# Kernel tuning notes

Measured on AMD Instinct MI355X. Metric: run time of the kernel, lower is better.

## Reference

```python
import jax, jax.numpy as jnp
import numpy as np
from jax import lax

N = 5000          # num atoms
E = 4             # num edge types
DIM_H = 128
VOCAB = 100       # num_atoms_vocab; embedding table has VOCAB+1 rows
T = 4             # max_time_steps


def setup_inputs() -> dict:
    key = jax.random.key(0)
    k1, k2, k3, k4 = jax.random.split(key, 4)
    atom_arr = jax.random.randint(k1, (N,), 0, VOCAB, dtype=jnp.int64 if jax.config.read('jax_enable_x64') else jnp.int32)
    adjs = jax.random.randint(k2, (E, N, N), 0, 2, dtype=jnp.int32)
    # learned parameters
    embedding = jax.random.normal(k3, (VOCAB + 1, DIM_H), dtype=jnp.float32) * 0.05
    limit = float(np.sqrt(6.0 / (DIM_H + DIM_H)))  # glorot uniform
    H_edges = jax.random.uniform(k4, (E, DIM_H, DIM_H), minval=-limit, maxval=limit, dtype=jnp.float32)
    return {
        "atom_arr": atom_arr,
        "adjs": adjs,
        "max_time_steps": T,
        "embedding": embedding,
        "H_edges": H_edges,
    }


def reference(atom_arr, adjs, max_time_steps, embedding, H_edges):
    # h_v^0 = embedding lookup, [N, H]
    h0 = embedding[atom_arr]
    # adjacency mask as float, [E, N, N]
    A = (adjs == 1).astype(h0.dtype)

    def step(h, _):
        # original: for each node v, edge type e: H_e @ sum_{u: adj[e,v,u]==1} h_u
        agg = jnp.einsum('evu,uh->evh', A, h)          # neighbor sum per edge type
        msg = jnp.einsum('eij,evj->vi', H_edges, agg)  # edge-type transform + sum over e
        h_new = jax.nn.sigmoid(h + msg)
        return h_new, h_new

    _, h_all = lax.scan(step, h0, None, length=max_time_steps)
    return h_all  # [T, N, H]
```

## Files before the change

### kernel.cpp

```cpp
#include <hip/hip_runtime.h>

#define NROW 5000
#define NPAD 5120
#define KPAD 5120
#define KW   80
#define KC   80
#define KZ   4
#define KCQ  20
#define HDIM 128
#define MTI  5
#define MROWS (MTI * 32)
#define FXS  4194304.0f
#define PART ((size_t)4 * NROW * HDIM)

typedef _Float16 f16x8 __attribute__((ext_vector_type(8)));
typedef float f32x16 __attribute__((ext_vector_type(16)));

__device__ __forceinline__ unsigned short f2h_int(int v) {
    union { _Float16 h; unsigned short u; } c;
    c.h = (_Float16)(float)v;
    return c.u;
}
__device__ __forceinline__ void fx_digits(float h, unsigned short& d1, unsigned short& d0) {
    int q = (int)rintf(h * FXS);
    d1 = f2h_int(q >> 11);
    d0 = f2h_int(q & 2047);
}

__device__ __forceinline__ size_t bt_idx(int kc, int pl, int kk, int half, int col, int j) {
    return (((((size_t)kc * 2 + pl) * 4 + kk) * 2 + half) * 128 + col) * 8 + j;
}

__global__ __launch_bounds__(256) void prep_atom_kernel(const unsigned int* __restrict__ atomw,
                                                        int* __restrict__ atomIdx) {
    __shared__ int s_is64;
    if (threadIdx.x == 0) {
        bool all0 = true, anynz = false;
        for (int j = 0; j < 64; ++j) {
            unsigned lo = atomw[2 * j], hi = atomw[2 * j + 1];
            all0 = all0 && (hi == 0u);
            anynz = anynz || (lo != 0u);
        }
        s_is64 = (all0 && anynz) ? 1 : 0;
    }
    __syncthreads();
    int v = blockIdx.x * 256 + threadIdx.x;
    if (v < NROW) atomIdx[v] = s_is64 ? (int)atomw[2 * v] : (int)atomw[v];
}

__global__ __launch_bounds__(256) void prep_pack_kernel(const int* __restrict__ adjs,
                                                        unsigned long long* __restrict__ packedT) {
    const int er = blockIdx.x;
    const int e = er / NPAD;
    const int r = er - e * NPAD;
    const int wave = threadIdx.x >> 6;
    const int lane = threadIdx.x & 63;
    const int* rowp = adjs + ((size_t)e * NROW + r) * NROW;
    unsigned long long* outp = packedT + (size_t)e * KC * NPAD + r;
    const bool rok = (r < NROW);
    for (int c = wave; c < KW; c += 4) {
        int u = c * 64 + lane;
        int val = (rok && u < NROW) ? rowp[u] : 0;
        unsigned long long m = __ballot(val == 1);
        if (lane == 0) outp[(size_t)c * NPAD] = m;
    }
}

__global__ __launch_bounds__(256) void prep_h0T_kernel(const int* __restrict__ atomIdx,
                                                       const float* __restrict__ emb,
                                                       unsigned short* __restrict__ hTt) {
    const int i = blockIdx.y;
    const int v = blockIdx.x * 256 + threadIdx.x;
    float val = 0.f;
    if (v < NROW) val = emb[(size_t)atomIdx[v] * HDIM + i];
    unsigned short d1, d0;
    fx_digits(val, d1, d0);
    const int kc = v >> 6, kk = (v >> 4) & 3, half = (v >> 3) & 1, j = v & 7;
    hTt[bt_idx(kc, 0, kk, half, i, j)] = d1;
    hTt[bt_idx(kc, 1, kk, half, i, j)] = d0;
}

__global__ __launch_bounds__(256) void prep_h0f_kernel(const int* __restrict__ atomIdx,
                                                       const float* __restrict__ emb,
                                                       float* __restrict__ h) {
    int idx = blockIdx.x * 256 + threadIdx.x;
    int v = idx >> 7, i = idx & 127;
    h[idx] = emb[(size_t)atomIdx[v] * HDIM + i];
}

__global__ __launch_bounds__(256) void prep_Ht_kernel(const float* __restrict__ H,
                                                      float* __restrict__ Htr) {
    int idx = blockIdx.x * 256 + threadIdx.x;
    int e = idx >> 14;
    int j = (idx >> 7) & 127;
    int i = idx & 127;
    Htr[idx] = H[((size_t)e * HDIM + i) * HDIM + j];
}

__global__ __launch_bounds__(256, 2) void gemm1_kernel(const unsigned long long* __restrict__ packedT,
                                                       const unsigned short* __restrict__ hTt,
                                                       float* __restrict__ agg) {
    const int m0 = blockIdx.x * MROWS;
    const int e = blockIdx.y;
    const int kz = blockIdx.z;
    const int tid = threadIdx.x;
    const int lane = tid & 63;
    const int wave = tid >> 6;
    const int l31 = lane & 31;
    const int l1 = lane >> 5;
    const int sh2 = l1 * 8;
    const int col = wave * 32 + l31;

    f32x16 acc[2][MTI];
#pragma unroll
    for (int pl = 0; pl < 2; ++pl)
#pragma unroll
        for (int mt = 0; mt < MTI; ++mt) acc[pl][mt] = (f32x16)(0.f);

    const int kc0 = kz * KCQ;
    const unsigned long long* ap = packedT + ((size_t)e * KC + kc0) * NPAD + m0 + l31;
    const _Float16* bp = (const _Float16*)hTt + (size_t)kc0 * 16384 + (size_t)l1 * 1024 + (size_t)col * 8;

    for (int kc = 0; kc < KCQ; ++kc) {
        unsigned long long aw[MTI];
#pragma unroll
        for (int mt = 0; mt < MTI; ++mt) aw[mt] = ap[mt * 32];

        f16x8 bf[2][4];
#pragma unroll
        for (int pl = 0; pl < 2; ++pl)
#pragma unroll
            for (int kk = 0; kk < 4; ++kk)
                bf[pl][kk] = *(const f16x8*)(bp + pl * 8192 + kk * 2048);

        ap += NPAD;
        bp += 16384;

#pragma unroll
        for (int kk = 0; kk < 4; ++kk) {
#pragma unroll
            for (int mt = 0; mt < MTI; ++mt) {
                unsigned int w = (kk < 2) ? (unsigned int)aw[mt] : (unsigned int)(aw[mt] >> 32);
                unsigned int b = (w >> ((kk & 1) * 16 + sh2)) & 0xFFu;
                unsigned int y = b | (b << 15);
                union { unsigned int u[4]; f16x8 h; } A;
#pragma unroll
                for (int q = 0; q < 4; ++q)
                    A.u[q] = ((y >> (2 * q)) & 0x00010001u) * 0x3C00u;
#pragma unroll
                for (int pl = 0; pl < 2; ++pl)
                    acc[pl][mt] = __builtin_amdgcn_mfma_f32_32x32x16_f16(
                        A.h, bf[pl][kk], acc[pl][mt], 0, 0, 0);
            }
        }
    }

    float* aggz = agg + (size_t)kz * PART;
#pragma unroll
    for (int mt = 0; mt < MTI; ++mt)
#pragma unroll
        for (int reg = 0; reg < 16; ++reg) {
            int row = (reg & 3) + 8 * (reg >> 2) + 4 * l1;
            int v = m0 + mt * 32 + row;
            if (v < NROW) {
                double d = (double)acc[0][mt][reg] * 2048.0 + (double)acc[1][mt][reg];
                aggz[((size_t)e * NROW + v) * HDIM + col] = (float)(d * (1.0 / 4194304.0));
            }
        }
}

__global__ __launch_bounds__(256) void gemm2_kernel(const float* __restrict__ agg,
                                                    const float* __restrict__ Htr,
                                                    float* __restrict__ h,
                                                    float* __restrict__ outp,
                                                    unsigned short* __restrict__ hTt) {
    __shared__ float aggs[16][512];
    __shared__ unsigned short hs[2][128][16];
    const int v0 = blockIdx.x * 16;
    const int tid = threadIdx.x;

#pragma unroll
    for (int it = 0; it < 8; ++it) {
        int idx = it * 256 + tid;
        int vv = idx >> 7;
        int ej = (idx & 127) * 4;
        int e = ej >> 7, j = ej & 127;
        int v = v0 + vv;
        float4 val = make_float4(0.f, 0.f, 0.f, 0.f);
        if (v < NROW) {
            size_t o = ((size_t)e * NROW + v) * HDIM + j;
            float4 a0 = *(const float4*)&agg[o];
            float4 a1 = *(const float4*)&agg[PART + o];
            float4 a2 = *(const float4*)&agg[2 * PART + o];
            float4 a3 = *(const float4*)&agg[3 * PART + o];
            val = make_float4((a0.x + a1.x) + (a2.x + a3.x), (a0.y + a1.y) + (a2.y + a3.y),
                              (a0.z + a1.z) + (a2.z + a3.z), (a0.w + a1.w) + (a2.w + a3.w));
        }
        *(float4*)&aggs[vv][ej] = val;
    }
    __syncthreads();

    const int i = tid & 127;
    const int vg = tid >> 7;
    float m4[8][4];
#pragma unroll
    for (int vv = 0; vv < 8; ++vv)
#pragma unroll
        for (int k = 0; k < 4; ++k) m4[vv][k] = 0.f;

    for (int c = 0; c < 512; c += 4) {
        float w0 = Htr[(size_t)(c + 0) * HDIM + i];
        float w1 = Htr[(size_t)(c + 1) * HDIM + i];
        float w2 = Htr[(size_t)(c + 2) * HDIM + i];
        float w3 = Htr[(size_t)(c + 3) * HDIM + i];
#pragma unroll
        for (int vv = 0; vv < 8; ++vv) {
            const float4 a = *(const float4*)&aggs[vg * 8 + vv][c];
            m4[vv][0] += a.x * w0;
            m4[vv][1] += a.y * w1;
            m4[vv][2] += a.z * w2;
            m4[vv][3] += a.w * w3;
        }
    }

#pragma unroll
    for (int vv = 0; vv < 8; ++vv) {
        int v = v0 + vg * 8 + vv;
        unsigned short d1 = 0, d0 = 0;
        if (v < NROW) {
            size_t o = (size_t)v * HDIM + i;
            float msg = (m4[vv][0] + m4[vv][1]) + (m4[vv][2] + m4[vv][3]);
            float x = h[o] + msg;
            float s = 1.0f / (1.0f + expf(-x));
            outp[o] = s;
            h[o] = s;
            fx_digits(s, d1, d0);
        }
        hs[0][i][vg * 8 + vv] = d1;
        hs[1][i][vg * 8 + vv] = d0;
    }
    __syncthreads();
    if (tid < 128) {
        const int kc = v0 >> 6, kk = (v0 >> 4) & 3;
#pragma unroll
        for (int pl = 0; pl < 2; ++pl) {
            const uint4* sp = (const uint4*)&hs[pl][tid][0];
            *(uint4*)&hTt[bt_idx(kc, pl, kk, 0, tid, 0)] = sp[0];
            *(uint4*)&hTt[bt_idx(kc, pl, kk, 1, tid, 0)] = sp[1];
        }
    }
}

extern "C" void kernel_launch(void* const* d_in, const int* in_sizes, int n_in,
                              void* d_out, int out_size, void* d_ws, size_t ws_size,
                              hipStream_t stream) {
    const unsigned int* atomw = (const unsigned int*)d_in[0];
    const int* adjs = (const int*)d_in[1];
    const float* emb = (const float*)d_in[3];
    const float* H = (const float*)d_in[4];
    float* out = (float*)d_out;

    char* ws = (char*)d_ws;
    unsigned long long* packedT = (unsigned long long*)ws;
    size_t off = (size_t)4 * KC * NPAD * 8;
    unsigned short* hTt = (unsigned short*)(ws + off);
    off += (size_t)2 * KC * HDIM * 64 * 2;
    float* hf = (float*)(ws + off);
    off += (size_t)NROW * HDIM * 4;
    float* agg = (float*)(ws + off);
    off += (size_t)KZ * PART * 4;
    float* Htr = (float*)(ws + off);
    off += (size_t)4 * HDIM * HDIM * 4;
    int* atomIdx = (int*)(ws + off);
    off += (size_t)NROW * 4;

    prep_atom_kernel<<<dim3((NROW + 255) / 256), 256, 0, stream>>>(atomw, atomIdx);
    prep_pack_kernel<<<dim3(4 * NPAD), 256, 0, stream>>>(adjs, packedT);
    prep_h0T_kernel<<<dim3(KPAD / 256, HDIM), 256, 0, stream>>>(atomIdx, emb, hTt);
    prep_h0f_kernel<<<dim3(NROW * HDIM / 256), 256, 0, stream>>>(atomIdx, emb, hf);
    prep_Ht_kernel<<<dim3(4 * HDIM * HDIM / 256), 256, 0, stream>>>(H, Htr);

    for (int t = 0; t < 4; ++t) {
        gemm1_kernel<<<dim3(NPAD / MROWS, 4, KZ), 256, 0, stream>>>(packedT, hTt, agg);
        gemm2_kernel<<<dim3((NROW + 15) / 16), 256, 0, stream>>>(agg, Htr, hf,
                                                                 out + (size_t)t * NROW * HDIM, hTt);
    }
}
```

Before: 1.057 ms.

## Fuse time-step GEMM kernels into one persistent kernel with grid barriers

```diff
diff --git a/kernel.cpp b/kernel.cpp
--- a/kernel.cpp
+++ b/kernel.cpp
@@ -2,7 +2,6 @@
 
 #define NROW 5000
 #define NPAD 5120
-#define KPAD 5120
 #define KW   80
 #define KC   80
 #define KZ   4
@@ -10,6 +9,8 @@
 #define HDIM 128
 #define MTI  5
 #define MROWS (MTI * 32)
+#define GRID1 512
+#define NT2  625
 #define FXS  4194304.0f
 #define PART ((size_t)4 * NROW * HDIM)
 
@@ -31,8 +32,20 @@
     return (((((size_t)kc * 2 + pl) * 4 + kk) * 2 + half) * 128 + col) * 8 + j;
 }
 
+__device__ __forceinline__ void gridbar(int* bar, int idx) {
+    __syncthreads();
+    if (threadIdx.x == 0) {
+        __hip_atomic_fetch_add(&bar[idx], 1, __ATOMIC_ACQ_REL, __HIP_MEMORY_SCOPE_AGENT);
+        while (__hip_atomic_load(&bar[idx], __ATOMIC_ACQUIRE, __HIP_MEMORY_SCOPE_AGENT) < GRID1)
+            __builtin_amdgcn_s_sleep(2);
+    }
+    __syncthreads();
+}
+
 __global__ __launch_bounds__(256) void prep_atom_kernel(const unsigned int* __restrict__ atomw,
-                                                        int* __restrict__ atomIdx) {
+                                                        int* __restrict__ atomIdx,
+                                                        int* __restrict__ bar) {
+    if (blockIdx.x == 0 && threadIdx.x < 16) bar[threadIdx.x] = 0;
     __shared__ int s_is64;
     if (threadIdx.x == 0) {
         bool all0 = true, anynz = false;
@@ -97,157 +110,174 @@
     Htr[idx] = H[((size_t)e * HDIM + i) * HDIM + j];
 }
 
-__global__ __launch_bounds__(256, 2) void gemm1_kernel(const unsigned long long* __restrict__ packedT,
-                                                       const unsigned short* __restrict__ hTt,
-                                                       float* __restrict__ agg) {
-    const int m0 = blockIdx.x * MROWS;
-    const int e = blockIdx.y;
-    const int kz = blockIdx.z;
+__global__ __launch_bounds__(256, 2) void fused_kernel(const unsigned long long* __restrict__ packedT,
+                                                       unsigned short* __restrict__ hTt,
+                                                       float* __restrict__ agg,
+                                                       const float* __restrict__ Htr,
+                                                       float* __restrict__ hf,
+                                                       float* __restrict__ out,
+                                                       int* __restrict__ bar) {
+    __shared__ float aggs[8][512];
+    __shared__ unsigned short hs[2][128][8];
     const int tid = threadIdx.x;
+    const int bid = blockIdx.x;
+
+    const int mblk = bid & 31;
+    const int e1 = (bid >> 5) & 3;
+    const int kz = bid >> 7;
     const int lane = tid & 63;
     const int wave = tid >> 6;
     const int l31 = lane & 31;
     const int l1 = lane >> 5;
     const int sh2 = l1 * 8;
     const int col = wave * 32 + l31;
-
-    f32x16 acc[2][MTI];
-#pragma unroll
-    for (int pl = 0; pl < 2; ++pl)
-#pragma unroll
-        for (int mt = 0; mt < MTI; ++mt) acc[pl][mt] = (f32x16)(0.f);
-
+    const int m0 = mblk * MROWS;
     const int kc0 = kz * KCQ;
-    const unsigned long long* ap = packedT + ((size_t)e * KC + kc0) * NPAD + m0 + l31;
-    const _Float16* bp = (const _Float16*)hTt + (size_t)kc0 * 16384 + (size_t)l1 * 1024 + (size_t)col * 8;
-
-    for (int kc = 0; kc < KCQ; ++kc) {
-        unsigned long long aw[MTI];
-#pragma unroll
-        for (int mt = 0; mt < MTI; ++mt) aw[mt] = ap[mt * 32];
-
-        f16x8 bf[2][4];
-#pragma unroll
-        for (int pl = 0; pl < 2; ++pl)
-#pragma unroll
-            for (int kk = 0; kk < 4; ++kk)
-                bf[pl][kk] = *(const f16x8*)(bp + pl * 8192 + kk * 2048);
-
-        ap += NPAD;
-        bp += 16384;
-
-#pragma unroll
-        for (int kk = 0; kk < 4; ++kk) {
-#pragma unroll
-            for (int mt = 0; mt < MTI; ++mt) {
-                unsigned int w = (kk < 2) ? (unsigned int)aw[mt] : (unsigned int)(aw[mt] >> 32);
-                unsigned int b = (w >> ((kk & 1) * 16 + sh2)) & 0xFFu;
-                unsigned int y = b | (b << 15);
-                union { unsigned int u[4]; f16x8 h; } A;
-#pragma unroll
-                for (int q = 0; q < 4; ++q)
-                    A.u[q] = ((y >> (2 * q)) & 0x00010001u) * 0x3C00u;
+
+    const int ip = tid & 63;
+    const int vg = tid >> 6;
+    const int i0 = ip * 2;
+
+    for (int t = 0; t < 4; ++t) {
+        {
+            f32x16 acc[2][MTI];
+#pragma unroll
+            for (int pl = 0; pl < 2; ++pl)
+#pragma unroll
+                for (int mt = 0; mt < MTI; ++mt) acc[pl][mt] = (f32x16)(0.f);
+
+            const unsigned long long* ap = packedT + ((size_t)e1 * KC + kc0) * NPAD + m0 + l31;
+            const _Float16* bp = (const _Float16*)hTt + (size_t)kc0 * 16384 +
+                                 (size_t)l1 * 1024 + (size_t)col * 8;
+
+            for (int kc = 0; kc < KCQ; ++kc) {
+                unsigned long long aw[MTI];
+#pragma unroll
+                for (int mt = 0; mt < MTI; ++mt) aw[mt] = ap[mt * 32];
+
+                f16x8 bf[2][4];
 #pragma unroll
                 for (int pl = 0; pl < 2; ++pl)
-                    acc[pl][mt] = __builtin_amdgcn_mfma_f32_32x32x16_f16(
-                        A.h, bf[pl][kk], acc[pl][mt], 0, 0, 0);
-            }
+#pragma unroll
+                    for (int kk = 0; kk < 4; ++kk)
+                        bf[pl][kk] = *(const f16x8*)(bp + pl * 8192 + kk * 2048);
+
+                ap += NPAD;
+                bp += 16384;
+
+#pragma unroll
+                for (int kk = 0; kk < 4; ++kk) {
+#pragma unroll
+                    for (int mt = 0; mt < MTI; ++mt) {
+                        unsigned int w = (kk < 2) ? (unsigned int)aw[mt]
+                                                  : (unsigned int)(aw[mt] >> 32);
+                        unsigned int b = (w >> ((kk & 1) * 16 + sh2)) & 0xFFu;
+                        unsigned int y = b | (b << 15);
+                        union { unsigned int u[4]; f16x8 h; } A;
+#pragma unroll
+                        for (int q = 0; q < 4; ++q)
+                            A.u[q] = ((y >> (2 * q)) & 0x00010001u) * 0x3C00u;
+#pragma unroll
+                        for (int pl = 0; pl < 2; ++pl)
+                            acc[pl][mt] = __builtin_amdgcn_mfma_f32_32x32x16_f16(
+                                A.h, bf[pl][kk], acc[pl][mt], 0, 0, 0);
+                    }
+                }
+            }
+
+            float* aggz = agg + (size_t)kz * PART;
+#pragma unroll
+            for (int mt = 0; mt < MTI; ++mt)
+#pragma unroll
+                for (int reg = 0; reg < 16; ++reg) {
+                    int row = (reg & 3) + 8 * (reg >> 2) + 4 * l1;
+                    int v = m0 + mt * 32 + row;
+                    if (v < NROW) {
+                        double d = (double)acc[0][mt][reg] * 2048.0 + (double)acc[1][mt][reg];
+                        aggz[((size_t)e1 * NROW + v) * HDIM + col] = (float)(d * (1.0 / 4194304.0));
+                    }
+                }
         }
-    }
-
-    float* aggz = agg + (size_t)kz * PART;
-#pragma unroll
-    for (int mt = 0; mt < MTI; ++mt)
-#pragma unroll
-        for (int reg = 0; reg < 16; ++reg) {
-            int row = (reg & 3) + 8 * (reg >> 2) + 4 * l1;
-            int v = m0 + mt * 32 + row;
-            if (v < NROW) {
-                double d = (double)acc[0][mt][reg] * 2048.0 + (double)acc[1][mt][reg];
-                aggz[((size_t)e * NROW + v) * HDIM + col] = (float)(d * (1.0 / 4194304.0));
+        gridbar(bar, 2 * t);
+
+        float* outp = out + (size_t)t * NROW * HDIM;
+        for (int tile = bid; tile < NT2; tile += GRID1) {
+            const int v0 = tile * 8;
+#pragma unroll
+            for (int it = 0; it < 4; ++it) {
+                int idx = it * 256 + tid;
+                int r = idx >> 7;
+                int c = (idx & 127) * 4;
+                int e = c >> 7, j = c & 127;
+                size_t o = ((size_t)e * NROW + (v0 + r)) * HDIM + j;
+                float4 a0 = *(const float4*)&agg[o];
+                float4 a1 = *(const float4*)&agg[PART + o];
+                float4 a2 = *(const float4*)&agg[2 * PART + o];
+                float4 a3 = *(const float4*)&agg[3 * PART + o];
+                *(float4*)&aggs[r][c] = make_float4((a0.x + a1.x) + (a2.x + a3.x),
+                                                    (a0.y + a1.y) + (a2.y + a3.y),
+                                                    (a0.z + a1.z) + (a2.z + a3.z),
+                                                    (a0.w + a1.w) + (a2.w + a3.w));
+            }
+            __syncthreads();
+
+            float m[2][2][4];
+#pragma unroll
+            for (int r = 0; r < 2; ++r)
+#pragma unroll
+                for (int q = 0; q < 2; ++q)
+#pragma unroll
+                    for (int k = 0; k < 4; ++k) m[r][q][k] = 0.f;
+
+            const int rb = vg * 2;
+            for (int cg = 0; cg < 128; ++cg) {
+                int c = cg * 4;
+                float4 q0 = *(const float4*)&aggs[rb][c];
+                float4 q1 = *(const float4*)&aggs[rb + 1][c];
+                float a0v[4] = {q0.x, q0.y, q0.z, q0.w};
+                float a1v[4] = {q1.x, q1.y, q1.z, q1.w};
+#pragma unroll
+                for (int k = 0; k < 4; ++k) {
+                    float2 w = *(const float2*)&Htr[(size_t)(c + k) * HDIM + i0];
+                    m[0][0][k] += a0v[k] * w.x;
+                    m[0][1][k] += a0v[k] * w.y;
+                    m[1][0][k] += a1v[k] * w.x;
+                    m[1][1][k] += a1v[k] * w.y;
+                }
+            }
+
+#pragma unroll
+            for (int r = 0; r < 2; ++r) {
+                int vr = rb + r;
+                int v = v0 + vr;
+                size_t o = (size_t)v * HDIM + i0;
+                float2 hv = *(const float2*)&hf[o];
+                float ms0 = (m[r][0][0] + m[r][0][1]) + (m[r][0][2] + m[r][0][3]);
+                float ms1 = (m[r][1][0] + m[r][1][1]) + (m[r][1][2] + m[r][1][3]);
+                float x0 = hv.x + ms0;
+                float x1 = hv.y + ms1;
+                float s0 = 1.0f / (1.0f + expf(-x0));
+                float s1 = 1.0f / (1.0f + expf(-x1));
+                *(float2*)&outp[o] = make_float2(s0, s1);
+                *(float2*)&hf[o] = make_float2(s0, s1);
+                unsigned short d1a, d0a, d1b, d0b;
+                fx_digits(s0, d1a, d0a);
+                fx_digits(s1, d1b, d0b);
+                hs[0][i0][vr] = d1a;
+                hs[1][i0][vr] = d0a;
+                hs[0][i0 + 1][vr] = d1b;
+                hs[1][i0 + 1][vr] = d0b;
+            }
+            __syncthreads();
+            if (tid < 128) {
+                const int kc = v0 >> 6, kk = (v0 >> 4) & 3, half = (v0 >> 3) & 1;
+#pragma unroll
+                for (int pl = 0; pl < 2; ++pl)
+                    *(uint4*)&hTt[bt_idx(kc, pl, kk, half, tid, 0)] =
+                        *(const uint4*)&hs[pl][tid][0];
             }
         }
-}
-
-__global__ __launch_bounds__(256) void gemm2_kernel(const float* __restrict__ agg,
-                                                    const float* __restrict__ Htr,
-                                                    float* __restrict__ h,
-                                                    float* __restrict__ outp,
-                                                    unsigned short* __restrict__ hTt) {
-    __shared__ float aggs[16][512];
-    __shared__ unsigned short hs[2][128][16];
-    const int v0 = blockIdx.x * 16;
-    const int tid = threadIdx.x;
-
-#pragma unroll
-    for (int it = 0; it < 8; ++it) {
-        int idx = it * 256 + tid;
-        int vv = idx >> 7;
-        int ej = (idx & 127) * 4;
-        int e = ej >> 7, j = ej & 127;
-        int v = v0 + vv;
-        float4 val = make_float4(0.f, 0.f, 0.f, 0.f);
-        if (v < NROW) {
-            size_t o = ((size_t)e * NROW + v) * HDIM + j;
-            float4 a0 = *(const float4*)&agg[o];
-            float4 a1 = *(const float4*)&agg[PART + o];
-            float4 a2 = *(const float4*)&agg[2 * PART + o];
-            float4 a3 = *(const float4*)&agg[3 * PART + o];
-            val = make_float4((a0.x + a1.x) + (a2.x + a3.x), (a0.y + a1.y) + (a2.y + a3.y),
-                              (a0.z + a1.z) + (a2.z + a3.z), (a0.w + a1.w) + (a2.w + a3.w));
-        }
-        *(float4*)&aggs[vv][ej] = val;
-    }
-    __syncthreads();
-
-    const int i = tid & 127;
-    const int vg = tid >> 7;
-    float m4[8][4];
-#pragma unroll
-    for (int vv = 0; vv < 8; ++vv)
-#pragma unroll
-        for (int k = 0; k < 4; ++k) m4[vv][k] = 0.f;
-
-    for (int c = 0; c < 512; c += 4) {
-        float w0 = Htr[(size_t)(c + 0) * HDIM + i];
-        float w1 = Htr[(size_t)(c + 1) * HDIM + i];
-        float w2 = Htr[(size_t)(c + 2) * HDIM + i];
-        float w3 = Htr[(size_t)(c + 3) * HDIM + i];
-#pragma unroll
-        for (int vv = 0; vv < 8; ++vv) {
-            const float4 a = *(const float4*)&aggs[vg * 8 + vv][c];
-            m4[vv][0] += a.x * w0;
-            m4[vv][1] += a.y * w1;
-            m4[vv][2] += a.z * w2;
-            m4[vv][3] += a.w * w3;
-        }
-    }
-
-#pragma unroll
-    for (int vv = 0; vv < 8; ++vv) {
-        int v = v0 + vg * 8 + vv;
-        unsigned short d1 = 0, d0 = 0;
-        if (v < NROW) {
-            size_t o = (size_t)v * HDIM + i;
-            float msg = (m4[vv][0] + m4[vv][1]) + (m4[vv][2] + m4[vv][3]);
-            float x = h[o] + msg;
-            float s = 1.0f / (1.0f + expf(-x));
-            outp[o] = s;
-            h[o] = s;
-            fx_digits(s, d1, d0);
-        }
-        hs[0][i][vg * 8 + vv] = d1;
-        hs[1][i][vg * 8 + vv] = d0;
-    }
-    __syncthreads();
-    if (tid < 128) {
-        const int kc = v0 >> 6, kk = (v0 >> 4) & 3;
-#pragma unroll
-        for (int pl = 0; pl < 2; ++pl) {
-            const uint4* sp = (const uint4*)&hs[pl][tid][0];
-            *(uint4*)&hTt[bt_idx(kc, pl, kk, 0, tid, 0)] = sp[0];
-            *(uint4*)&hTt[bt_idx(kc, pl, kk, 1, tid, 0)] = sp[1];
-        }
+        if (t != 3) gridbar(bar, 2 * t + 1);
     }
 }
 
@@ -273,16 +303,15 @@
     off += (size_t)4 * HDIM * HDIM * 4;
     int* atomIdx = (int*)(ws + off);
     off += (size_t)NROW * 4;
-
-    prep_atom_kernel<<<dim3((NROW + 255) / 256), 256, 0, stream>>>(atomw, atomIdx);
+    off = (off + 63) & ~(size_t)63;
+    int* bar = (int*)(ws + off);
+    off += 64;
+
+    prep_atom_kernel<<<dim3((NROW + 255) / 256), 256, 0, stream>>>(atomw, atomIdx, bar);
     prep_pack_kernel<<<dim3(4 * NPAD), 256, 0, stream>>>(adjs, packedT);
-    prep_h0T_kernel<<<dim3(KPAD / 256, HDIM), 256, 0, stream>>>(atomIdx, emb, hTt);
+    prep_h0T_kernel<<<dim3(NPAD / 256, HDIM), 256, 0, stream>>>(atomIdx, emb, hTt);
     prep_h0f_kernel<<<dim3(NROW * HDIM / 256), 256, 0, stream>>>(atomIdx, emb, hf);
     prep_Ht_kernel<<<dim3(4 * HDIM * HDIM / 256), 256, 0, stream>>>(H, Htr);
 
-    for (int t = 0; t < 4; ++t) {
-        gemm1_kernel<<<dim3(NPAD / MROWS, 4, KZ), 256, 0, stream>>>(packedT, hTt, agg);
-        gemm2_kernel<<<dim3((NROW + 15) / 16), 256, 0, stream>>>(agg, Htr, hf,
-                                                                 out + (size_t)t * NROW * HDIM, hTt);
-    }
-}
+    fused_kernel<<<dim3(GRID1), 256, 0, stream>>>(packedT, hTt, agg, Htr, hf, out, bar);
+}
```

After: 2.340 ms. 121% more time.
